# Optimization experiments

Measured on AMD Instinct MI355X. Metric: run time of the kernel, lower is better.

## Reference

```python
import jax, jax.numpy as jnp
import numpy as np

NP = 44
B = 400000

def setup_inputs() -> dict:
    key = jax.random.key(0)
    ks = jax.random.split(key, 9)
    return {
        "X":    jax.random.normal(ks[0], (NP, 1, B), dtype=jnp.float32),
        "lin1": jax.random.normal(ks[1], (NP, 4, 1), dtype=jnp.float32),
        "lin2": jax.random.normal(ks[2], (NP, 8, 4), dtype=jnp.float32),
        "lin3": jax.random.normal(ks[3], (NP, 4, 8), dtype=jnp.float32),
        "lin4": jax.random.normal(ks[4], (NP, 1, 4), dtype=jnp.float32),
        "b1":   jax.random.normal(ks[5], (NP, 4, 1), dtype=jnp.float32),
        "b2":   jax.random.normal(ks[6], (NP, 8, 1), dtype=jnp.float32),
        "b3":   jax.random.normal(ks[7], (NP, 4, 1), dtype=jnp.float32),
        "b4":   jax.random.normal(ks[8], (NP, 1, 1), dtype=jnp.float32),
    }

def reference(X, lin1, lin2, lin3, lin4, b1, b2, b3, b4):
    # forward_all: three relu(W @ X + b) layers, then a final affine layer.
    # Batched over NP populations ('l'), broadcast over the huge sample dim ('j').
    h = jax.nn.relu(jnp.einsum('lik,lkj->lij', lin1, X) + b1)   # (NP, 4, B)
    h = jax.nn.relu(jnp.einsum('lik,lkj->lij', lin2, h) + b2)   # (NP, 8, B)
    h = jax.nn.relu(jnp.einsum('lik,lkj->lij', lin3, h) + b3)   # (NP, 4, B)
    out = jnp.einsum('lik,lkj->lij', lin4, h) + b4              # (NP, 1, B)
    return out
```

## Files before the change

### kernel.cpp

```cpp
#include <hip/hip_runtime.h>


#define NP 44
#define BATCH 400000
#define B4C (BATCH / 4)
#define GRIDX 49

typedef float v2f __attribute__((ext_vector_type(2)));
typedef float v4f __attribute__((ext_vector_type(4)));
typedef _Float16 h2 __attribute__((ext_vector_type(2)));

__device__ __forceinline__ h2 hsplat(float s) {
    _Float16 h = (_Float16)s;
    return (h2){h, h};
}

__device__ __forceinline__ h2 pk_cvt(float a, float b) {
    return __builtin_bit_cast(h2, __builtin_amdgcn_cvt_pkrtz(a, b));
}

__device__ __forceinline__ v2f mlp_pair(h2 x,
        const h2* __restrict__ w1, const h2* __restrict__ w2,
        const h2* __restrict__ w3, const h2* __restrict__ c1,
        const h2* __restrict__ c2, const h2* __restrict__ c3,
        const float* __restrict__ w4, float c4) {
    const h2 zero = (h2){(_Float16)0.0f, (_Float16)0.0f};
    h2 h1[4], t2[8], h3[4];
#pragma unroll
    for (int i = 0; i < 4; ++i) {
        h2 a = __builtin_elementwise_fma(w1[i], x, c1[i]);
        h1[i] = __builtin_elementwise_max(a, zero);
    }
#pragma unroll
    for (int i = 0; i < 8; ++i) {
        h2 a = c2[i];
#pragma unroll
        for (int k = 0; k < 4; ++k)
            a = __builtin_elementwise_fma(w2[i * 4 + k], h1[k], a);
        t2[i] = __builtin_elementwise_max(a, zero);
    }
#pragma unroll
    for (int i = 0; i < 4; ++i) {
        h2 a = c3[i];
#pragma unroll
        for (int k = 0; k < 8; ++k)
            a = __builtin_elementwise_fma(w3[i * 8 + k], t2[k], a);
        h3[i] = __builtin_elementwise_max(a, zero);
    }
    float o0 = c4, o1 = c4;
#pragma unroll
    for (int k = 0; k < 4; ++k) {
        o0 = fmaf(w4[k], (float)h3[k].x, o0);
        o1 = fmaf(w4[k], (float)h3[k].y, o1);
    }
    return (v2f){o0, o1};
}

__global__ __launch_bounds__(256) void mlp_fwd_kernel(
        const float* __restrict__ X,
        const float* __restrict__ lin1,
        const float* __restrict__ lin2,
        const float* __restrict__ lin3,
        const float* __restrict__ lin4,
        const float* __restrict__ b1,
        const float* __restrict__ b2,
        const float* __restrict__ b3,
        const float* __restrict__ b4,
        float* __restrict__ out) {
    const int l = blockIdx.y;

    h2 w1[4], c1[4], w2[32], c2[8], w3[32], c3[4];
    float w4[4];
#pragma unroll
    for (int i = 0; i < 4; ++i) {
        w1[i] = hsplat(lin1[l * 4 + i]);
        c1[i] = hsplat(b1[l * 4 + i]);
        c3[i] = hsplat(b3[l * 4 + i]);
        w4[i] = lin4[l * 4 + i];
    }
#pragma unroll
    for (int i = 0; i < 32; ++i) {
        w2[i] = hsplat(lin2[l * 32 + i]);
        w3[i] = hsplat(lin3[l * 32 + i]);
    }
#pragma unroll
    for (int i = 0; i < 8; ++i)
        c2[i] = hsplat(b2[l * 8 + i]);
    const float c4 = b4[l];

    const v4f* __restrict__ xin = (const v4f*)(X + (size_t)l * BATCH);
    v4f* po = (v4f*)(out + (size_t)l * BATCH);

    for (int j4 = blockIdx.x * blockDim.x + threadIdx.x; j4 < B4C;
         j4 += GRIDX * 256) {
        v4f x = xin[j4];
        h2 xa = pk_cvt(x.x, x.y);
        h2 xb = pk_cvt(x.z, x.w);
        v2f p0 = mlp_pair(xa, w1, w2, w3, c1, c2, c3, w4, c4);
        v2f p1 = mlp_pair(xb, w1, w2, w3, c1, c2, c3, w4, c4);
        v4f r = (v4f){p0.x, p0.y, p1.x, p1.y};
        __builtin_nontemporal_store(r, po + j4);
    }
}

extern "C" void kernel_launch(void* const* d_in, const int* in_sizes, int n_in,
                              void* d_out, int out_size, void* d_ws, size_t ws_size,
                              hipStream_t stream) {
    const float* X    = (const float*)d_in[0];
    const float* lin1 = (const float*)d_in[1];
    const float* lin2 = (const float*)d_in[2];
    const float* lin3 = (const float*)d_in[3];
    const float* lin4 = (const float*)d_in[4];
    const float* b1   = (const float*)d_in[5];
    const float* b2   = (const float*)d_in[6];
    const float* b3   = (const float*)d_in[7];
    const float* b4   = (const float*)d_in[8];
    float* out = (float*)d_out;

    dim3 block(256);
    dim3 grid(GRIDX, NP);
    mlp_fwd_kernel<<<grid, block, 0, stream>>>(X, lin1, lin2, lin3, lin4,
                                               b1, b2, b3, b4, out);
}
```

Measured before the change: 144.2 us.

## Precompute packed half-precision weights in a prep kernel and unroll two items per thread

A tiny prep kernel converts each population's weights and biases into packed fp16 splats in workspace once per call. The main kernel then loads these pre-packed words instead of converting per block. The grid-stride loop is replaced by a fixed grid of 196x44 blocks, with each thread handling two float4 elements whose loads are issued up front. The cost is an extra kernel launch and serialisation between the two kernels.

```diff
diff --git a/kernel.cpp b/kernel.cpp
--- a/kernel.cpp
+++ b/kernel.cpp
@@ -4,19 +4,50 @@
 #define NP 44
 #define BATCH 400000
 #define B4C (BATCH / 4)
-#define GRIDX 49
+#define BLOCKS_X 196
+#define PP_DW 96
 
 typedef float v2f __attribute__((ext_vector_type(2)));
 typedef float v4f __attribute__((ext_vector_type(4)));
 typedef _Float16 h2 __attribute__((ext_vector_type(2)));
 
-__device__ __forceinline__ h2 hsplat(float s) {
-    _Float16 h = (_Float16)s;
-    return (h2){h, h};
+__device__ __forceinline__ unsigned int splat_u(float s) {
+    unsigned short h = __builtin_bit_cast(unsigned short, (_Float16)s);
+    return ((unsigned int)h << 16) | (unsigned int)h;
 }
 
 __device__ __forceinline__ h2 pk_cvt(float a, float b) {
     return __builtin_bit_cast(h2, __builtin_amdgcn_cvt_pkrtz(a, b));
+}
+
+__global__ void prep_kernel(const float* __restrict__ lin1,
+                            const float* __restrict__ lin2,
+                            const float* __restrict__ lin3,
+                            const float* __restrict__ lin4,
+                            const float* __restrict__ b1,
+                            const float* __restrict__ b2,
+                            const float* __restrict__ b3,
+                            const float* __restrict__ b4,
+                            unsigned int* __restrict__ ws) {
+    const int l = threadIdx.x;
+    if (l >= NP) return;
+    unsigned int* o = ws + l * PP_DW;
+#pragma unroll
+    for (int i = 0; i < 4; ++i)  o[i]      = splat_u(lin1[l * 4 + i]);
+#pragma unroll
+    for (int i = 0; i < 32; ++i) o[4 + i]  = splat_u(lin2[l * 32 + i]);
+#pragma unroll
+    for (int i = 0; i < 32; ++i) o[36 + i] = splat_u(lin3[l * 32 + i]);
+#pragma unroll
+    for (int i = 0; i < 4; ++i)  o[68 + i] = splat_u(b1[l * 4 + i]);
+#pragma unroll
+    for (int i = 0; i < 8; ++i)  o[72 + i] = splat_u(b2[l * 8 + i]);
+#pragma unroll
+    for (int i = 0; i < 4; ++i)  o[80 + i] = splat_u(b3[l * 4 + i]);
+    float* of = (float*)(o + 84);
+#pragma unroll
+    for (int i = 0; i < 4; ++i)  of[i] = lin4[l * 4 + i];
+    of[4] = b4[l];
 }
 
 __device__ __forceinline__ v2f mlp_pair(h2 x,
@@ -58,48 +89,51 @@
 
 __global__ __launch_bounds__(256) void mlp_fwd_kernel(
         const float* __restrict__ X,
-        const float* __restrict__ lin1,
-        const float* __restrict__ lin2,
-        const float* __restrict__ lin3,
-        const float* __restrict__ lin4,
-        const float* __restrict__ b1,
-        const float* __restrict__ b2,
-        const float* __restrict__ b3,
-        const float* __restrict__ b4,
+        const unsigned int* __restrict__ ws,
         float* __restrict__ out) {
     const int l = blockIdx.y;
+    const unsigned int* p = ws + l * PP_DW;
 
-    h2 w1[4], c1[4], w2[32], c2[8], w3[32], c3[4];
+    h2 w1[4], w2[32], w3[32], c1[4], c2[8], c3[4];
     float w4[4];
 #pragma unroll
-    for (int i = 0; i < 4; ++i) {
-        w1[i] = hsplat(lin1[l * 4 + i]);
-        c1[i] = hsplat(b1[l * 4 + i]);
-        c3[i] = hsplat(b3[l * 4 + i]);
-        w4[i] = lin4[l * 4 + i];
-    }
+    for (int i = 0; i < 4; ++i)  w1[i] = __builtin_bit_cast(h2, p[i]);
 #pragma unroll
-    for (int i = 0; i < 32; ++i) {
-        w2[i] = hsplat(lin2[l * 32 + i]);
-        w3[i] = hsplat(lin3[l * 32 + i]);
-    }
+    for (int i = 0; i < 32; ++i) w2[i] = __builtin_bit_cast(h2, p[4 + i]);
 #pragma unroll
-    for (int i = 0; i < 8; ++i)
-        c2[i] = hsplat(b2[l * 8 + i]);
-    const float c4 = b4[l];
+    for (int i = 0; i < 32; ++i) w3[i] = __builtin_bit_cast(h2, p[36 + i]);
+#pragma unroll
+    for (int i = 0; i < 4; ++i)  c1[i] = __builtin_bit_cast(h2, p[68 + i]);
+#pragma unroll
+    for (int i = 0; i < 8; ++i)  c2[i] = __builtin_bit_cast(h2, p[72 + i]);
+#pragma unroll
+    for (int i = 0; i < 4; ++i)  c3[i] = __builtin_bit_cast(h2, p[80 + i]);
+    const float* pf = (const float*)(p + 84);
+#pragma unroll
+    for (int i = 0; i < 4; ++i)  w4[i] = pf[i];
+    const float c4 = pf[4];
 
     const v4f* __restrict__ xin = (const v4f*)(X + (size_t)l * BATCH);
     v4f* po = (v4f*)(out + (size_t)l * BATCH);
 
-    for (int j4 = blockIdx.x * blockDim.x + threadIdx.x; j4 < B4C;
-         j4 += GRIDX * 256) {
-        v4f x = xin[j4];
-        h2 xa = pk_cvt(x.x, x.y);
-        h2 xb = pk_cvt(x.z, x.w);
-        v2f p0 = mlp_pair(xa, w1, w2, w3, c1, c2, c3, w4, c4);
-        v2f p1 = mlp_pair(xb, w1, w2, w3, c1, c2, c3, w4, c4);
-        v4f r = (v4f){p0.x, p0.y, p1.x, p1.y};
-        __builtin_nontemporal_store(r, po + j4);
+    const int j4a = blockIdx.x * 512 + threadIdx.x;
+    const int j4b = j4a + 256;
+    const bool va = j4a < B4C;
+    const bool vb = j4b < B4C;
+
+    v4f x0, x1;
+    if (va) x0 = xin[j4a];
+    if (vb) x1 = xin[j4b];
+
+    if (va) {
+        v2f p0 = mlp_pair(pk_cvt(x0.x, x0.y), w1, w2, w3, c1, c2, c3, w4, c4);
+        v2f p1 = mlp_pair(pk_cvt(x0.z, x0.w), w1, w2, w3, c1, c2, c3, w4, c4);
+        __builtin_nontemporal_store((v4f){p0.x, p0.y, p1.x, p1.y}, po + j4a);
+    }
+    if (vb) {
+        v2f p0 = mlp_pair(pk_cvt(x1.x, x1.y), w1, w2, w3, c1, c2, c3, w4, c4);
+        v2f p1 = mlp_pair(pk_cvt(x1.z, x1.w), w1, w2, w3, c1, c2, c3, w4, c4);
+        __builtin_nontemporal_store((v4f){p0.x, p0.y, p1.x, p1.y}, po + j4b);
     }
 }
 
@@ -116,9 +150,11 @@
     const float* b3   = (const float*)d_in[7];
     const float* b4   = (const float*)d_in[8];
     float* out = (float*)d_out;
+    unsigned int* ws = (unsigned int*)d_ws;
+
+    prep_kernel<<<1, 64, 0, stream>>>(lin1, lin2, lin3, lin4, b1, b2, b3, b4, ws);
 
     dim3 block(256);
-    dim3 grid(GRIDX, NP);
-    mlp_fwd_kernel<<<grid, block, 0, stream>>>(X, lin1, lin2, lin3, lin4,
-                                               b1, b2, b3, b4, out);
+    dim3 grid(BLOCKS_X, NP);
+    mlp_fwd_kernel<<<grid, block, 0, stream>>>(X, ws, out);
 }
```

After: 144.6 us. About the same (+0.3%).
